# Optimization experiments

Measured on AMD Instinct MI355X. Metric: run time of the kernel, lower is better.

The kernel has to match this reference:

```python
import jax, jax.numpy as jnp
import numpy as np

_D4_CODESZ = 4
_NUM_SCALE = 1024.0


def _code3_signs(i3, x):
    if i3 & (1 << 5):
        x[2] *= -1
    if i3 & (1 << 6):
        x[1] *= -1
    if sum(x) % 2 != 0:
        x[3] *= -1
    if i3 & (1 << 7):
        x = [-v for v in x]
    assert sum(x) % 2 == 0
    return x


def _code8_to_d4(i8):
    assert 0 <= i8 < 256
    i3 = i8 & (7 << 5)
    i8 = i8 & 31
    if i8 < 16:
        if i8 < 8:
            if i8 < 2:
                if i8 < 1:
                    return _code3_signs(i3, [0.5] * _D4_CODESZ)
                else:
                    return _code3_signs(i3, [1.5] * _D4_CODESZ)
            else:
                ibx = i8 >> 1
                if i8 & 1:
                    x = [0.5] * _D4_CODESZ
                    x[0] = 1.5
                    x[ibx] = 1.5
                else:
                    x = [1.5] * _D4_CODESZ
                    x[0] = 0.5
                    x[ibx] = 0.5
                return _code3_signs(i3, x)
        else:
            ibx = i8 & 3
            if i8 < 8 + 4:
                x = [0.5] * _D4_CODESZ
                x[ibx] = 1.5
            else:
                x = [1.5] * _D4_CODESZ
                x[ibx] = 0.5
            return _code3_signs(i3, x)
    elif i8 < 16 + 4:
        ibx = i8 & 3
        x = [0.5] * _D4_CODESZ
        x[ibx] = 2.5
        return _code3_signs(i3, x)
    else:
        ibx = i8 - 20
        ib4 = ibx & 3
        ib3 = ibx >> 2
        x = [0.5] * _D4_CODESZ
        x[ib4] = 1.5
        if ib3 >= ib4:
            ib3 += 1
        x[ib3] = 2.5
        return _code3_signs(i3, x)


def build_d4_cb():
    cb = np.zeros((256, _D4_CODESZ), dtype=np.float32)
    for i in range(256):
        cb[i] = _code8_to_d4(i)
    return jnp.asarray(cb, dtype=jnp.float16)


def fwht(x):
    """Normalized fast Walsh-Hadamard transform over the last axis (power of 2).
    The normalized Hadamard matrix is symmetric, so U and U^T coincide."""
    shp = x.shape
    n = shp[-1]
    x = x.reshape(-1, n)
    h = 1
    while h < n:
        x = x.reshape(-1, n // (2 * h), 2, h)
        a = x[:, :, 0, :]
        b = x[:, :, 1, :]
        x = jnp.stack([a + b, a - b], axis=2).reshape(-1, n)
        h *= 2
    return (x * np.float32(1.0 / np.sqrt(n))).reshape(shp)


def setup_inputs() -> dict:
    key = jax.random.key(0)
    k1, k2, k3, k4, k5 = jax.random.split(key, 5)
    m, n = 4096, 1024  # out_features=m, in_features=4*n
    d_in = _D4_CODESZ * n
    inp = {
        "input": jax.random.normal(k1, (4, 2048, d_in), dtype=jnp.float32),
        "Qidxs": jax.random.randint(k2, (m, n), 0, 256, dtype=jnp.int32),
        "SU": jnp.sign(jax.random.normal(k3, (d_in,), dtype=jnp.float32)),
        "SV": jnp.sign(jax.random.normal(k4, (m,), dtype=jnp.float32)),
        "Wscale": jax.random.uniform(k5, (1,), dtype=jnp.float32) + 0.5,
        "D4_CB": build_d4_cb(),
    }
    return inp


def reference(input, Qidxs, SU, SV, Wscale, D4_CB):
    m, n = Qidxs.shape
    d_in = _D4_CODESZ * n
    x = input.reshape(-1, d_in).astype(jnp.float32)  # [T, 4n]
    x = x * SU                                        # sign diag
    x = fwht(x)                                       # AutogradOrthoMult, transpose=1
    x = (x / _NUM_SCALE).astype(jnp.float16)
    # on-the-fly D4 dequant: gather codebook rows, fuse into GEMM
    W = D4_CB[Qidxs].reshape(m, d_in)                 # [m, 4n] fp16
    z = x @ W.T                                       # [T, m] fp16 (AutogradQuip)
    x = z.astype(jnp.float32) * (Wscale * _NUM_SCALE)
    x = fwht(x)                                       # AutogradOrthoMult, transpose=0
    x = x * SV                                        # sign diag
    return x.reshape(input.shape[:-1] + (m,))
```

## Files before the change

kernel.cpp:

```cpp
#include <hip/hip_runtime.h>
#include <hip/hip_fp16.h>

typedef _Float16 half8 __attribute__((ext_vector_type(8)));
typedef _Float16 half4v __attribute__((ext_vector_type(4)));
typedef float floatx4 __attribute__((ext_vector_type(4)));

#define K_DIM 4096
#define N_DIM 4096
#define B_ROWS 8192

#define BM 256
#define BN 256
#define BK 64
#define NTILES (K_DIM / BK)

__global__ __launch_bounds__(256) void decode_kernel(
    const int2* __restrict__ qidxs, const float4* __restrict__ cb,
    half8* __restrict__ w) {
  int i = blockIdx.x * 256 + threadIdx.x;
  int2 q = qidxs[i];
  float4 v0 = cb[q.x];
  float4 v1 = cb[q.y];
  half8 h;
  h[0] = (_Float16)v0.x;
  h[1] = (_Float16)v0.y;
  h[2] = (_Float16)v0.z;
  h[3] = (_Float16)v0.w;
  h[4] = (_Float16)v1.x;
  h[5] = (_Float16)v1.y;
  h[6] = (_Float16)v1.z;
  h[7] = (_Float16)v1.w;
  w[i] = h;
}

__device__ __forceinline__ void fwht16(float v[16]) {
#pragma unroll
  for (int h = 1; h < 16; h <<= 1) {
#pragma unroll
    for (int g = 0; g < 16; g += 2 * h) {
#pragma unroll
      for (int j = g; j < g + h; ++j) {
        float a = v[j], b = v[j + h];
        v[j] = a + b;
        v[j + h] = a - b;
      }
    }
  }
}

__global__ __launch_bounds__(256) void fwht_in_kernel(
    const float* __restrict__ x, const float* __restrict__ su,
    _Float16* __restrict__ out) {
  __shared__ float s[16][264];
  const int t = threadIdx.x;
  const float* xr = x + (size_t)blockIdx.x * 4096;
  float v[16];
#pragma unroll
  for (int a = 0; a < 16; ++a) v[a] = xr[a * 256 + t] * su[a * 256 + t];
  fwht16(v);
  {
    const int c = t >> 4, d = t & 15;
    const int col = c * 16 + (d ^ c);
#pragma unroll
    for (int a = 0; a < 16; ++a) s[a][col] = v[a];
  }
  __syncthreads();
  const int a0 = t >> 4, d0 = t & 15;
#pragma unroll
  for (int c = 0; c < 16; ++c) v[c] = s[a0][c * 16 + (d0 ^ c)];
  fwht16(v);
#pragma unroll
  for (int c = 0; c < 16; ++c) s[a0][c * 16 + (d0 ^ c)] = v[c];
  __syncthreads();
  const int c1 = t & 15;
#pragma unroll
  for (int d = 0; d < 16; ++d) v[d] = s[a0][c1 * 16 + (d ^ c1)];
  fwht16(v);
  const float sc = 1.0f / 65536.0f;
  half8 h0, h1;
#pragma unroll
  for (int d = 0; d < 8; ++d) h0[d] = (_Float16)(v[d] * sc);
#pragma unroll
  for (int d = 0; d < 8; ++d) h1[d] = (_Float16)(v[d + 8] * sc);
  half8* ov = (half8*)(out + (size_t)blockIdx.x * 4096 + t * 16);
  ov[0] = h0;
  ov[1] = h1;
}

__device__ __forceinline__ void gload16(const _Float16* g, _Float16* l) {
  __builtin_amdgcn_global_load_lds(
      (const __attribute__((address_space(1))) void*)g,
      (__attribute__((address_space(3))) void*)l, 16, 0, 0);
}

#define MF(a, b, c) __builtin_amdgcn_mfma_f32_16x16x32_f16(a, b, c, 0, 0, 0)

#define LDA(BUFI, M, KS) \
  (*(const half8*)&sA[BUFI][wm * 128 + (M) * 16 + fr][fc ^ ((KS) << 5)])
#define LDB(BUFI, Nn, KS) \
  (*(const half8*)&sB[BUFI][wn * 64 + (Nn) * 16 + fr][fc ^ ((KS) << 5)])

#define STAGE_A(BUFI, HALF, TILE)                                            \
  {                                                                          \
    const _Float16* s_ = gA + (long)(HALF) * 128 * K_DIM + (long)(TILE)*BK;  \
    _Float16* d_ = &sA[BUFI][(HALF)*128 + sr][scl];                          \
    gload16(s_, d_);                                                         \
    gload16(s_ + 64 * (long)K_DIM, d_ + 64 * BK);                            \
  }
#define STAGE_B(BUFI, HALF, TILE)                                            \
  {                                                                          \
    const _Float16* s_ = gB + (long)(HALF) * 128 * K_DIM + (long)(TILE)*BK;  \
    _Float16* d_ = &sB[BUFI][(HALF)*128 + sr][scl];                          \
    gload16(s_, d_);                                                         \
    gload16(s_ + 64 * (long)K_DIM, d_ + 64 * BK);                            \
  }

#define WAIT4 asm volatile("s_waitcnt vmcnt(4)" ::: "memory")
#define WAIT0 asm volatile("s_waitcnt vmcnt(0)" ::: "memory")

#define PHASE(BUFI, M0, STAGE_STMT, TAIL_STMT)                               \
  {                                                                          \
    half8 x00 = LDA(BUFI, M0, 0);                                            \
    half8 x01 = LDA(BUFI, M0, 1);                                            \
    half8 x10 = LDA(BUFI, (M0) + 1, 0);                                      \
    half8 x11 = LDA(BUFI, (M0) + 1, 1);                                      \
    STAGE_STMT;                                                              \
    __builtin_amdgcn_s_barrier();                                            \
    asm volatile("s_waitcnt lgkmcnt(0)" ::: "memory");                       \
    __builtin_amdgcn_sched_barrier(0);                                       \
    __builtin_amdgcn_s_setprio(1);                                           \
    acc[M0][0] = MF(x00, bf[0][0], acc[M0][0]);                              \
    acc[M0][1] = MF(x00, bf[1][0], acc[M0][1]);                              \
    acc[M0][2] = MF(x00, bf[2][0], acc[M0][2]);                              \
    acc[M0][3] = MF(x00, bf[3][0], acc[M0][3]);                              \
    acc[(M0) + 1][0] = MF(x10, bf[0][0], acc[(M0) + 1][0]);                  \
    acc[(M0) + 1][1] = MF(x10, bf[1][0], acc[(M0) + 1][1]);                  \
    acc[(M0) + 1][2] = MF(x10, bf[2][0], acc[(M0) + 1][2]);                  \
    acc[(M0) + 1][3] = MF(x10, bf[3][0], acc[(M0) + 1][3]);                  \
    acc[M0][0] = MF(x01, bf[0][1], acc[M0][0]);                              \
    acc[M0][1] = MF(x01, bf[1][1], acc[M0][1]);                              \
    acc[M0][2] = MF(x01, bf[2][1], acc[M0][2]);                              \
    acc[M0][3] = MF(x01, bf[3][1], acc[M0][3]);                              \
    acc[(M0) + 1][0] = MF(x11, bf[0][1], acc[(M0) + 1][0]);                  \
    acc[(M0) + 1][1] = MF(x11, bf[1][1], acc[(M0) + 1][1]);                  \
    acc[(M0) + 1][2] = MF(x11, bf[2][1], acc[(M0) + 1][2]);                  \
    acc[(M0) + 1][3] = MF(x11, bf[3][1], acc[(M0) + 1][3]);                  \
    __builtin_amdgcn_s_setprio(0);                                           \
    TAIL_STMT;                                                               \
    __builtin_amdgcn_s_barrier();                                            \
  }

#define TILE(BUFI, S1, S2, S3, S4, TAILW)                                    \
  {                                                                          \
    half8 bf[4][2];                                                          \
    bf[0][0] = LDB(BUFI, 0, 0);                                              \
    bf[0][1] = LDB(BUFI, 0, 1);                                              \
    bf[1][0] = LDB(BUFI, 1, 0);                                              \
    bf[1][1] = LDB(BUFI, 1, 1);                                              \
    bf[2][0] = LDB(BUFI, 2, 0);                                              \
    bf[2][1] = LDB(BUFI, 2, 1);                                              \
    bf[3][0] = LDB(BUFI, 3, 0);                                              \
    bf[3][1] = LDB(BUFI, 3, 1);                                              \
    PHASE(BUFI, 0, S1, ;)                                                    \
    PHASE(BUFI, 2, S2, ;)                                                    \
    PHASE(BUFI, 4, S3, ;)                                                    \
    PHASE(BUFI, 6, S4, TAILW)                                                \
  }

__global__ __launch_bounds__(512) void gemm_kernel(
    const _Float16* __restrict__ A,
    const _Float16* __restrict__ B,
    float* __restrict__ C) {
  __shared__ _Float16 sA[2][BM][BK];
  __shared__ _Float16 sB[2][BN][BK];
  const int t = threadIdx.x;
  const int lane = t & 63;
  const int wave = t >> 6;
  const int wm = wave >> 2;
  const int wn = wave & 3;

  const int bid = blockIdx.x;
  const int wg = (bid & 7) * 64 + (bid >> 3);
  const long bm = (long)(wg >> 4) * BM;
  const long bn = (long)(wg & 15) * BN;

  floatx4 acc[8][4];
#pragma unroll
  for (int i = 0; i < 8; i++)
#pragma unroll
    for (int j = 0; j < 4; j++) acc[i][j] = floatx4{0.f, 0.f, 0.f, 0.f};

  const int sr = t >> 3;
  const int scl = (t & 7) << 3;
  const int sc = ((t & 7) ^ (sr & 7)) << 3;
  const _Float16* gA = A + (bm + sr) * (long)K_DIM + sc;
  const _Float16* gB = B + (bn + sr) * (long)K_DIM + sc;

  const int fr = lane & 15;
  const int fc = (((lane >> 4) ^ (lane & 7)) << 3);

  STAGE_A(0, 0, 0);
  STAGE_A(0, 1, 0);
  STAGE_B(0, 0, 0);
  STAGE_B(0, 1, 0);
  STAGE_B(1, 0, 1);
  STAGE_B(1, 1, 1);
  WAIT4;
  __builtin_amdgcn_s_barrier();

#pragma unroll 1
  for (int kt = 0; kt < NTILES - 2; kt += 2) {
    TILE(0, STAGE_A(1, 0, kt + 1), STAGE_A(1, 1, kt + 1),
         STAGE_B(0, 0, kt + 2), STAGE_B(0, 1, kt + 2), WAIT4)
    TILE(1, STAGE_A(0, 0, kt + 2), STAGE_A(0, 1, kt + 2),
         STAGE_B(1, 0, kt + 3), STAGE_B(1, 1, kt + 3), WAIT4)
  }
  TILE(0, STAGE_A(1, 0, NTILES - 1), STAGE_A(1, 1, NTILES - 1), ;, ;, WAIT0)
  TILE(1, ;, ;, ;, ;, ;)

  const int cn = lane & 15;
  const int cm4 = (lane >> 4) << 2;
#pragma unroll
  for (int m = 0; m < 8; m++) {
    const long row0 = bm + wm * 128 + m * 16 + cm4;
#pragma unroll
    for (int n = 0; n < 4; n++) {
      const long col = bn + wn * 64 + n * 16 + cn;
#pragma unroll
      for (int r = 0; r < 4; r++)
        C[(row0 + r) * (long)N_DIM + col] = (float)(_Float16)acc[m][n][r];
    }
  }
}

__global__ __launch_bounds__(256) void fwht_out_kernel(
    float* __restrict__ z, const float* __restrict__ sv,
    const float* __restrict__ wscale) {
  __shared__ float s[16][264];
  const int t = threadIdx.x;
  float* zr = z + (size_t)blockIdx.x * 4096;
  float v[16];
#pragma unroll
  for (int a = 0; a < 16; ++a) v[a] = zr[a * 256 + t];
  fwht16(v);
  {
    const int c = t >> 4, d = t & 15;
    const int col = c * 16 + (d ^ c);
#pragma unroll
    for (int a = 0; a < 16; ++a) s[a][col] = v[a];
  }
  __syncthreads();
  const int a0 = t >> 4, d0 = t & 15;
#pragma unroll
  for (int c = 0; c < 16; ++c) v[c] = s[a0][c * 16 + (d0 ^ c)];
  fwht16(v);
#pragma unroll
  for (int c = 0; c < 16; ++c) s[a0][c * 16 + (d0 ^ c)] = v[c];
  __syncthreads();
  const int c1 = t & 15;
#pragma unroll
  for (int d = 0; d < 16; ++d) v[d] = s[a0][c1 * 16 + (d ^ c1)];
  fwht16(v);
  const float scv = wscale[0] * 16.0f;
  const float4* svv = (const float4*)(sv + t * 16);
  float4* zo = (float4*)(zr + t * 16);
#pragma unroll
  for (int q = 0; q < 4; ++q) {
    float4 u = svv[q];
    float4 o;
    o.x = v[4 * q + 0] * scv * u.x;
    o.y = v[4 * q + 1] * scv * u.y;
    o.z = v[4 * q + 2] * scv * u.z;
    o.w = v[4 * q + 3] * scv * u.w;
    zo[q] = o;
  }
}

extern "C" void kernel_launch(void* const* d_in, const int* in_sizes, int n_in,
                              void* d_out, int out_size, void* d_ws, size_t ws_size,
                              hipStream_t stream) {
  const float* input = (const float*)d_in[0];
  const int* qidxs = (const int*)d_in[1];
  const float* su = (const float*)d_in[2];
  const float* sv = (const float*)d_in[3];
  const float* wscale = (const float*)d_in[4];
  const float4* cb = (const float4*)d_in[5];
  float* out = (float*)d_out;

  if (ws_size < 100663296ull) return;
  char* ws = (char*)d_ws;
  _Float16* W16 = (_Float16*)ws;
  _Float16* Xh = (_Float16*)(ws + 33554432ull);

  decode_kernel<<<(4096 * 1024 / 2) / 256, 256, 0, stream>>>(
      (const int2*)qidxs, cb, (half8*)W16);
  fwht_in_kernel<<<B_ROWS, 256, 0, stream>>>(input, su, Xh);
  gemm_kernel<<<dim3((B_ROWS / BM) * (N_DIM / BN)), 512, 0, stream>>>(Xh, W16,
                                                                      out);
  fwht_out_kernel<<<B_ROWS, 256, 0, stream>>>(out, sv, wscale);
}
```

Baseline: 508.1 us.

## Write fp16 GEMM output via LDS staging and vectorize FWHT loads

The GEMM epilogue can now store fp16 results, staged through a swizzled LDS patch so that each row is written with 16-byte coalesced stores into a workspace buffer. The output FWHT then reads fp16 instead of fp32, which halves the intermediate traffic. The FWHT kernels are also restructured into a 3-pass shared-memory transform with contiguous per-thread float4 loads instead of strided scalar loads. The fp16 path only runs if the workspace holds at least 160MB and otherwise falls back to the fp32 path.

```diff
diff --git a/kernel.cpp b/kernel.cpp
--- a/kernel.cpp
+++ b/kernel.cpp
@@ -2,7 +2,6 @@
 #include <hip/hip_fp16.h>
 
 typedef _Float16 half8 __attribute__((ext_vector_type(8)));
-typedef _Float16 half4v __attribute__((ext_vector_type(4)));
 typedef float floatx4 __attribute__((ext_vector_type(4)));
 
 #define K_DIM 4096
@@ -48,34 +47,47 @@
   }
 }
 
+__device__ __forceinline__ void fwht4096(float v[16], float* s, int t) {
+  const int a0 = t >> 4, c0 = t & 15;
+  fwht16(v);
+#pragma unroll
+  for (int d = 0; d < 16; ++d) s[a0 * 265 + c0 * 16 + (d ^ c0)] = v[d];
+  __syncthreads();
+  const int d1 = t & 15;
+#pragma unroll
+  for (int c = 0; c < 16; ++c) v[c] = s[a0 * 265 + c * 16 + (d1 ^ c)];
+  fwht16(v);
+#pragma unroll
+  for (int c = 0; c < 16; ++c) s[a0 * 265 + c * 16 + (d1 ^ c)] = v[c];
+  __syncthreads();
+  const int c2 = t >> 4, d2 = t & 15;
+#pragma unroll
+  for (int a = 0; a < 16; ++a) v[a] = s[a * 265 + c2 * 16 + (d2 ^ c2)];
+  fwht16(v);
+#pragma unroll
+  for (int a = 0; a < 16; ++a) s[a * 265 + c2 * 16 + (d2 ^ c2)] = v[a];
+  __syncthreads();
+#pragma unroll
+  for (int d = 0; d < 16; ++d) v[d] = s[a0 * 265 + c0 * 16 + (d ^ c0)];
+}
+
 __global__ __launch_bounds__(256) void fwht_in_kernel(
     const float* __restrict__ x, const float* __restrict__ su,
     _Float16* __restrict__ out) {
-  __shared__ float s[16][264];
+  __shared__ float s[16 * 265];
   const int t = threadIdx.x;
-  const float* xr = x + (size_t)blockIdx.x * 4096;
+  const float4* xv = (const float4*)(x + (size_t)blockIdx.x * 4096 + t * 16);
+  const float4* uv = (const float4*)(su + t * 16);
   float v[16];
 #pragma unroll
-  for (int a = 0; a < 16; ++a) v[a] = xr[a * 256 + t] * su[a * 256 + t];
-  fwht16(v);
-  {
-    const int c = t >> 4, d = t & 15;
-    const int col = c * 16 + (d ^ c);
-#pragma unroll
-    for (int a = 0; a < 16; ++a) s[a][col] = v[a];
-  }
-  __syncthreads();
-  const int a0 = t >> 4, d0 = t & 15;
-#pragma unroll
-  for (int c = 0; c < 16; ++c) v[c] = s[a0][c * 16 + (d0 ^ c)];
-  fwht16(v);
-#pragma unroll
-  for (int c = 0; c < 16; ++c) s[a0][c * 16 + (d0 ^ c)] = v[c];
-  __syncthreads();
-  const int c1 = t & 15;
-#pragma unroll
-  for (int d = 0; d < 16; ++d) v[d] = s[a0][c1 * 16 + (d ^ c1)];
-  fwht16(v);
+  for (int q = 0; q < 4; ++q) {
+    float4 a = xv[q], b = uv[q];
+    v[4 * q + 0] = a.x * b.x;
+    v[4 * q + 1] = a.y * b.y;
+    v[4 * q + 2] = a.z * b.z;
+    v[4 * q + 3] = a.w * b.w;
+  }
+  fwht4096(v, s, t);
   const float sc = 1.0f / 65536.0f;
   half8 h0, h1;
 #pragma unroll
@@ -167,10 +179,11 @@
     PHASE(BUFI, 6, S4, TAILW)                                                \
   }
 
+template <bool OUT_F16>
 __global__ __launch_bounds__(512) void gemm_kernel(
     const _Float16* __restrict__ A,
     const _Float16* __restrict__ B,
-    float* __restrict__ C) {
+    void* __restrict__ C) {
   __shared__ _Float16 sA[2][BM][BK];
   __shared__ _Float16 sB[2][BN][BK];
   const int t = threadIdx.x;
@@ -220,50 +233,80 @@
 
   const int cn = lane & 15;
   const int cm4 = (lane >> 4) << 2;
-#pragma unroll
-  for (int m = 0; m < 8; m++) {
-    const long row0 = bm + wm * 128 + m * 16 + cm4;
-#pragma unroll
-    for (int n = 0; n < 4; n++) {
-      const long col = bn + wn * 64 + n * 16 + cn;
-#pragma unroll
-      for (int r = 0; r < 4; r++)
-        C[(row0 + r) * (long)N_DIM + col] = (float)(_Float16)acc[m][n][r];
+  if (OUT_F16) {
+    __syncthreads();
+    _Float16* patch =
+        ((wave < 4) ? (_Float16*)sA : (_Float16*)sB) + (wave & 3) * 8192;
+#pragma unroll
+    for (int m = 0; m < 8; m++)
+#pragma unroll
+      for (int n = 0; n < 4; n++)
+#pragma unroll
+        for (int r = 0; r < 4; r++) {
+          int rl = m * 16 + cm4 + r, cl = n * 16 + cn;
+          patch[rl * 64 + (((cl >> 3) ^ (rl & 7)) << 3) + (cl & 7)] =
+              (_Float16)acc[m][n][r];
+        }
+    asm volatile("s_waitcnt lgkmcnt(0)" ::: "memory");
+    __builtin_amdgcn_sched_barrier(0);
+    _Float16* Co = (_Float16*)C;
+#pragma unroll
+    for (int p = 0; p < 16; p++) {
+      int rl = p * 8 + (lane >> 3);
+      int c8 = lane & 7;
+      half8 val = *(const half8*)(patch + rl * 64 + ((c8 ^ (rl & 7)) << 3));
+      *(half8*)(Co + (bm + wm * 128 + rl) * (long)N_DIM + bn + wn * 64 +
+                c8 * 8) = val;
     }
-  }
-}
-
+  } else {
+    float* Cf = (float*)C;
+#pragma unroll
+    for (int m = 0; m < 8; m++) {
+      const long row0 = bm + wm * 128 + m * 16 + cm4;
+#pragma unroll
+      for (int n = 0; n < 4; n++) {
+        const long col = bn + wn * 64 + n * 16 + cn;
+#pragma unroll
+        for (int r = 0; r < 4; r++)
+          Cf[(row0 + r) * (long)N_DIM + col] = (float)(_Float16)acc[m][n][r];
+      }
+    }
+  }
+}
+
+template <bool F16IN>
 __global__ __launch_bounds__(256) void fwht_out_kernel(
-    float* __restrict__ z, const float* __restrict__ sv,
-    const float* __restrict__ wscale) {
-  __shared__ float s[16][264];
+    const void* __restrict__ zin, float* __restrict__ zout,
+    const float* __restrict__ sv, const float* __restrict__ wscale) {
+  __shared__ float s[16 * 265];
   const int t = threadIdx.x;
-  float* zr = z + (size_t)blockIdx.x * 4096;
   float v[16];
-#pragma unroll
-  for (int a = 0; a < 16; ++a) v[a] = zr[a * 256 + t];
-  fwht16(v);
-  {
-    const int c = t >> 4, d = t & 15;
-    const int col = c * 16 + (d ^ c);
-#pragma unroll
-    for (int a = 0; a < 16; ++a) s[a][col] = v[a];
-  }
-  __syncthreads();
-  const int a0 = t >> 4, d0 = t & 15;
-#pragma unroll
-  for (int c = 0; c < 16; ++c) v[c] = s[a0][c * 16 + (d0 ^ c)];
-  fwht16(v);
-#pragma unroll
-  for (int c = 0; c < 16; ++c) s[a0][c * 16 + (d0 ^ c)] = v[c];
-  __syncthreads();
-  const int c1 = t & 15;
-#pragma unroll
-  for (int d = 0; d < 16; ++d) v[d] = s[a0][c1 * 16 + (d ^ c1)];
-  fwht16(v);
+  if (F16IN) {
+    const half8* zv =
+        (const half8*)((const _Float16*)zin + (size_t)blockIdx.x * 4096 +
+                       t * 16);
+    half8 h0 = zv[0], h1 = zv[1];
+#pragma unroll
+    for (int d = 0; d < 8; ++d) v[d] = (float)h0[d];
+#pragma unroll
+    for (int d = 0; d < 8; ++d) v[d + 8] = (float)h1[d];
+  } else {
+    const float4* zv =
+        (const float4*)((const float*)zin + (size_t)blockIdx.x * 4096 +
+                        t * 16);
+#pragma unroll
+    for (int q = 0; q < 4; ++q) {
+      float4 a = zv[q];
+      v[4 * q + 0] = a.x;
+      v[4 * q + 1] = a.y;
+      v[4 * q + 2] = a.z;
+      v[4 * q + 3] = a.w;
+    }
+  }
+  fwht4096(v, s, t);
   const float scv = wscale[0] * 16.0f;
   const float4* svv = (const float4*)(sv + t * 16);
-  float4* zo = (float4*)(zr + t * 16);
+  float4* zo = (float4*)(zout + (size_t)blockIdx.x * 4096 + t * 16);
 #pragma unroll
   for (int q = 0; q < 4; ++q) {
     float4 u = svv[q];
@@ -277,8 +320,8 @@
 }
 
 extern "C" void kernel_launch(void* const* d_in, const int* in_sizes, int n_in,
-                              void* d_out, int out_size, void* d_ws, size_t ws_size,
-                              hipStream_t stream) {
+                              void* d_out, int out_size, void* d_ws,
+                              size_t ws_size, hipStream_t stream) {
   const float* input = (const float*)d_in[0];
   const int* qidxs = (const int*)d_in[1];
   const float* su = (const float*)d_in[2];
@@ -291,11 +334,21 @@
   char* ws = (char*)d_ws;
   _Float16* W16 = (_Float16*)ws;
   _Float16* Xh = (_Float16*)(ws + 33554432ull);
+  _Float16* Zh = (_Float16*)(ws + 100663296ull);
+  const bool f16path = ws_size >= 167772160ull;
 
   decode_kernel<<<(4096 * 1024 / 2) / 256, 256, 0, stream>>>(
       (const int2*)qidxs, cb, (half8*)W16);
   fwht_in_kernel<<<B_ROWS, 256, 0, stream>>>(input, su, Xh);
-  gemm_kernel<<<dim3((B_ROWS / BM) * (N_DIM / BN)), 512, 0, stream>>>(Xh, W16,
-                                                                      out);
-  fwht_out_kernel<<<B_ROWS, 256, 0, stream>>>(out, sv, wscale);
-}
+  if (f16path) {
+    gemm_kernel<true><<<dim3((B_ROWS / BM) * (N_DIM / BN)), 512, 0, stream>>>(
+        Xh, W16, (void*)Zh);
+    fwht_out_kernel<true><<<B_ROWS, 256, 0, stream>>>((const void*)Zh, out, sv,
+                                                      wscale);
+  } else {
+    gemm_kernel<false><<<dim3((B_ROWS / BM) * (N_DIM / BN)), 512, 0, stream>>>(
+        Xh, W16, (void*)out);
+    fwht_out_kernel<false><<<B_ROWS, 256, 0, stream>>>((const void*)out, out,
+                                                       sv, wscale);
+  }
+}
```

Result: no change. 501.6 us (-1.3%).
